# Optimization experiments

Measured on AMD Instinct MI355X. Metric: run time of the kernel, lower is better.

Reference implementation:

```python
import jax, jax.numpy as jnp
import numpy as np

TOP_K = 2


def setup_inputs() -> dict:
    key = jax.random.key(0)
    k1, k2, k3, k4 = jax.random.split(key, 4)
    B, N, D, E, F = 4, 2048, 1024, 8, 4096
    x = jax.random.normal(k1, (B, N, D), dtype=jnp.float32)
    gate_w = jax.random.normal(k2, (D, E), dtype=jnp.float32) * (D ** -0.5)
    w1 = jax.random.normal(k3, (E, D, F), dtype=jnp.float32) * (D ** -0.5)
    w2 = jax.random.normal(k4, (E, F, D), dtype=jnp.float32) * (F ** -0.5)
    return {"x": x, "gate_w": gate_w, "w1": w1, "w2": w2}


def reference(x, gate_w, w1, w2):
    # x: (B, N, D); gate_w: (D, E); w1: (E, D, F); w2: (E, F, D)
    E = gate_w.shape[-1]
    gate_logits = jnp.einsum("bnd,de->bne", x, gate_w)
    gate_probs = jax.nn.softmax(gate_logits, axis=-1)          # (B, N, E)
    top_k_probs, top_k_idx = jax.lax.top_k(gate_probs, TOP_K)   # (B, N, K)
    top_k_weights = top_k_probs / jnp.sum(top_k_probs, axis=-1, keepdims=True)
    # combined per-expert weight: sum_k w_k * onehot(idx_k) -> (B, N, E)
    comb = jnp.sum(jax.nn.one_hot(top_k_idx, E, dtype=x.dtype)
                   * top_k_weights[..., None], axis=2)
    # dense all-expert FFN (matches the torch masked-dense math exactly)
    h = jax.nn.gelu(jnp.einsum("bnd,edf->benf", x, w1))         # (B, E, N, F)
    expert_out = jnp.einsum("benf,efd->bend", h, w2)            # (B, E, N, D)
    output = jnp.einsum("bne,bend->bnd", comb, expert_out)      # (B, N, D)
    return output
```

## Files before the change

### kernel.cpp

```cpp
#include <hip/hip_runtime.h>
#include <hip/hip_bf16.h>

typedef short s16x8 __attribute__((ext_vector_type(8)));
typedef float f32x4 __attribute__((ext_vector_type(4)));
typedef float f32x2 __attribute__((ext_vector_type(2)));
typedef unsigned short us8 __attribute__((ext_vector_type(8)));
typedef unsigned short us4 __attribute__((ext_vector_type(4)));

#define T_TOK 8192
#define DDIM 1024
#define NEXP 8
#define FDIM 4096
#define MAXT 72
#define PADMAX (16384 + NEXP * 256)

#define GLOAD16(dst, src) \
  __builtin_amdgcn_global_load_lds((const __attribute__((address_space(1))) unsigned int*)(src), \
                                   (__attribute__((address_space(3))) unsigned int*)(dst), 16, 0, 0)
#define WAITVM(n) asm volatile("s_waitcnt vmcnt(" #n ")" ::: "memory")
#define MEMFENCE asm volatile("" ::: "memory")

__device__ __forceinline__ float gelu_fast(float x) {
  float x2 = x * x;
  float t = x * fmaf(x2, -0.07135532f, -1.5957691f);
  float e = __expf(t);
  return x * __builtin_amdgcn_rcpf(1.0f + e);
}
__device__ __forceinline__ float bf2f(unsigned short v) {
  return __uint_as_float((unsigned)v << 16);
}

__global__ __launch_bounds__(256) void gate_kernel(
    const float* __restrict__ x, const float* __restrict__ gw,
    int* __restrict__ tok_e, float* __restrict__ tok_w)
{
  int lane = threadIdx.x & 63;
  int tok = blockIdx.x * 4 + (threadIdx.x >> 6);
  const float* xr = x + (size_t)tok * DDIM;
  float acc[NEXP];
#pragma unroll
  for (int e = 0; e < NEXP; ++e) acc[e] = 0.f;
  for (int i = 0; i < DDIM / 64; ++i) {
    int d = i * 64 + lane;
    float xv = xr[d];
    const float* g = gw + (size_t)d * NEXP;
#pragma unroll
    for (int e = 0; e < NEXP; ++e) acc[e] += xv * g[e];
  }
#pragma unroll
  for (int off = 32; off > 0; off >>= 1) {
#pragma unroll
    for (int e = 0; e < NEXP; ++e) acc[e] += __shfl_xor(acc[e], off);
  }
  if (lane == 0) {
    int i1 = 0; float m1 = acc[0];
#pragma unroll
    for (int e = 1; e < NEXP; ++e) if (acc[e] > m1) { m1 = acc[e]; i1 = e; }
    int i2 = -1; float m2 = -3.4e38f;
#pragma unroll
    for (int e = 0; e < NEXP; ++e) if (e != i1 && acc[e] > m2) { m2 = acc[e]; i2 = e; }
    float w1 = 1.f / (1.f + expf(m2 - m1));
    tok_e[tok * 2] = i1; tok_e[tok * 2 + 1] = i2;
    tok_w[tok * 2] = w1; tok_w[tok * 2 + 1] = 1.f - w1;
  }
}

__global__ __launch_bounds__(256) void count_kernel(
    const int* __restrict__ tok_e, int* __restrict__ counts)
{
  __shared__ int lc[NEXP];
  if (threadIdx.x < NEXP) lc[threadIdx.x] = 0;
  __syncthreads();
  int tok = blockIdx.x * 256 + threadIdx.x;
  atomicAdd(&lc[tok_e[tok * 2]], 1);
  atomicAdd(&lc[tok_e[tok * 2 + 1]], 1);
  __syncthreads();
  if (threadIdx.x < NEXP) atomicAdd(&counts[threadIdx.x], lc[threadIdx.x]);
}

__global__ void scan_kernel(const int* __restrict__ counts, int* padded_off,
                            int* tile_e, int* tile_row, int* numTiles,
                            int* __restrict__ pair_token)
{
  if (blockIdx.x == 0) {
    for (int i = threadIdx.x; i < PADMAX; i += 256) pair_token[i] = -1;
    if (threadIdx.x == 0) {
      int off = 0, a = 0;
      for (int e = 0; e < NEXP; ++e) {
        padded_off[e] = off;
        int c = counts[e];
        int nt = (c + 255) / 256;
        for (int i = 0; i < nt; ++i) { tile_e[a] = e; tile_row[a] = off + i * 256; ++a; }
        off += nt * 256;
      }
      *numTiles = a;
    }
  }
}

__global__ __launch_bounds__(256) void scatter_kernel(
    const int* __restrict__ tok_e, const int* __restrict__ padded_off,
    int* __restrict__ fill, int* __restrict__ pair_token, int* __restrict__ tok_slot)
{
  __shared__ int lc[NEXP], lbase[NEXP];
  if (threadIdx.x < NEXP) lc[threadIdx.x] = 0;
  __syncthreads();
  int tok = blockIdx.x * 256 + threadIdx.x;
  int e0 = tok_e[tok * 2], e1 = tok_e[tok * 2 + 1];
  int r0 = atomicAdd(&lc[e0], 1);
  int r1 = atomicAdd(&lc[e1], 1);
  __syncthreads();
  if (threadIdx.x < NEXP) lbase[threadIdx.x] = atomicAdd(&fill[threadIdx.x], lc[threadIdx.x]);
  __syncthreads();
  int s0 = padded_off[e0] + lbase[e0] + r0;
  int s1 = padded_off[e1] + lbase[e1] + r1;
  pair_token[s0] = tok;
  pair_token[s1] = tok;
  tok_slot[tok * 2] = s0;
  tok_slot[tok * 2 + 1] = s1;
}

__global__ __launch_bounds__(256) void gather_x(
    const float* __restrict__ x, const int* __restrict__ pair_token,
    __hip_bfloat16* __restrict__ Xg)
{
  int gid = blockIdx.x * 256 + threadIdx.x;
  int r = gid >> 7;
  int c = (gid & 127) << 3;
  if (r >= PADMAX) return;
  int tk = pair_token[r];
  __hip_bfloat16 v[8];
  if (tk < 0) {
#pragma unroll
    for (int j = 0; j < 8; ++j) v[j] = __float2bfloat16(0.f);
  } else {
    const float* src = x + (size_t)tk * DDIM + c;
    f32x4 a = __builtin_nontemporal_load((const f32x4*)src);
    f32x4 b = __builtin_nontemporal_load((const f32x4*)(src + 4));
#pragma unroll
    for (int j = 0; j < 4; ++j) v[j] = __float2bfloat16(a[j]);
#pragma unroll
    for (int j = 0; j < 4; ++j) v[4 + j] = __float2bfloat16(b[j]);
  }
  *(us8*)(Xg + (size_t)r * DDIM + c) = *(const us8*)v;
}

__global__ __launch_bounds__(256) void transpose_conv(
    const float* __restrict__ in, __hip_bfloat16* __restrict__ out, int R, int C)
{
  __shared__ __hip_bfloat16 tile[64][66];
  size_t mat = (size_t)R * C;
  const float* ip = in + (size_t)blockIdx.z * mat;
  __hip_bfloat16* op = out + (size_t)blockIdx.z * mat;
  int c0 = blockIdx.x * 64, r0 = blockIdx.y * 64;
  int tx = threadIdx.x & 31, ty = threadIdx.x >> 5;
#pragma unroll
  for (int i = 0; i < 8; ++i) {
    int r = r0 + ty + i * 8;
    f32x2 v = __builtin_nontemporal_load(
        (const f32x2*)(ip + (size_t)r * C + c0 + tx * 2));
    tile[ty + i * 8][tx * 2]     = __float2bfloat16(v[0]);
    tile[ty + i * 8][tx * 2 + 1] = __float2bfloat16(v[1]);
  }
  __syncthreads();
#pragma unroll
  for (int i = 0; i < 8; ++i) {
    int cc = c0 + ty + i * 8;
    __hip_bfloat16 a = tile[tx * 2][ty + i * 8];
    __hip_bfloat16 b = tile[tx * 2 + 1][ty + i * 8];
    unsigned short ua = *(unsigned short*)&a, ub = *(unsigned short*)&b;
    unsigned int packed = (unsigned)ua | ((unsigned)ub << 16);
    *(unsigned int*)(op + (size_t)cc * R + r0 + tx * 2) = packed;
  }
}

template<int LD, int NT, int LDO, int NCOL, int SC, bool GELU>
__global__ __launch_bounds__(512, 2) void moe_gemm8(
    const __hip_bfloat16* __restrict__ A, const __hip_bfloat16* __restrict__ B,
    __hip_bfloat16* __restrict__ Out,
    const int* __restrict__ tile_e, const int* __restrict__ tile_row,
    const int* __restrict__ numTiles)
{
  constexpr int STU = 3 * SC;
  constexpr int NCG = NCOL / SC;
  const int bid = blockIdx.x;
  const int xcd = bid & 7;
  const int idx = bid >> 3;
  const int stg = idx / STU;
  const int within = idx % STU;
  const int colg = stg % NCG;
  const int tg = stg / NCG;
  const int tl = tg * 3 + within % 3;
  const int col = colg * SC + within / 3;
  const int nT = *numTiles;
  const int tile = ((xcd * nT) >> 3) + tl;
  if (tile >= (((xcd + 1) * nT) >> 3)) return;

  __shared__ __align__(16) __hip_bfloat16 lds[8][8192];
  const int t = threadIdx.x, lane = t & 63, w = t >> 6;
  const int wm = w >> 2, wn = w & 3;
  const int fr = lane & 15, fkg = lane >> 4;
  const size_t rowoff = (size_t)(w * 8 + (lane >> 3)) * LD + (((lane & 7) ^ (lane >> 3)) << 3);
  const int aoff = (wm * 64 + fr) * 64;
  const int boff = (wn * 32 + fr) * 64;
  const int swk0 = (fkg ^ (fr & 7)) * 8;
  const int swk1 = ((4 + fkg) ^ (fr & 7)) * 8;

  const int e = tile_e[tile];
  const int row0 = tile_row[tile];
  const int col0 = col * 256;
  const __hip_bfloat16* Ab = A + (size_t)row0 * LD;
  const __hip_bfloat16* Bb = B + (size_t)e * ((size_t)FDIM * DDIM) + (size_t)col0 * LD;

  auto STAGEH = [&](const __hip_bfloat16* base, int mat, int half, int tt) {
    __hip_bfloat16* d = &lds[(((tt & 1) << 2) | (mat << 1) | half)][0] + w * 512;
    const __hip_bfloat16* s = base + (size_t)(half * 128) * LD + (size_t)tt * 64 + rowoff;
    GLOAD16(d, s);
    GLOAD16(d + 4096, s + (size_t)64 * LD);
  };

  f32x4 acc[4][4][2] = {};
  s16x8 af0[4][2], af1[4][2], b0[2][2], b1[2][2];

  STAGEH(Ab, 0, 0, 0); STAGEH(Bb, 1, 0, 0); STAGEH(Bb, 1, 1, 0); STAGEH(Ab, 0, 1, 0);
  STAGEH(Ab, 0, 0, 1);
  WAITVM(6);
  __builtin_amdgcn_s_barrier();
  MEMFENCE;
  {
    const __hip_bfloat16* A0r = &lds[0][0];
    const __hip_bfloat16* B0r = &lds[2][0];
#pragma unroll
    for (int m = 0; m < 4; ++m) {
      af0[m][0] = *(const s16x8*)(A0r + aoff + m * 1024 + swk0);
      af0[m][1] = *(const s16x8*)(A0r + aoff + m * 1024 + swk1);
    }
#pragma unroll
    for (int n = 0; n < 2; ++n) {
      b0[n][0] = *(const s16x8*)(B0r + boff + n * 1024 + swk0);
      b0[n][1] = *(const s16x8*)(B0r + boff + n * 1024 + swk1);
    }
  }

  for (int kt = 0; kt < NT; ++kt) {
    const int buf = kt & 1;
    const bool p1 = (kt + 1) < NT;
    const bool p2 = (kt + 2) < NT;
    const __hip_bfloat16* A1r = &lds[(buf << 2) | 1][0];
    const __hip_bfloat16* B1r = &lds[(buf << 2) | 3][0];
    const __hip_bfloat16* A0n = &lds[((buf ^ 1) << 2) | 0][0];
    const __hip_bfloat16* B0n = &lds[((buf ^ 1) << 2) | 2][0];

    if (p1) STAGEH(Bb, 1, 0, kt + 1);
    if (p1) { WAITVM(6); } else { WAITVM(2); }
    __builtin_amdgcn_s_barrier();
    MEMFENCE;
#pragma unroll
    for (int n = 0; n < 2; ++n) {
      b1[n][0] = *(const s16x8*)(B1r + boff + n * 1024 + swk0);
      b1[n][1] = *(const s16x8*)(B1r + boff + n * 1024 + swk1);
    }
    __builtin_amdgcn_s_setprio(1);
#pragma unroll
    for (int kk = 0; kk < 2; ++kk)
#pragma unroll
      for (int m = 0; m < 4; ++m)
#pragma unroll
        for (int n = 0; n < 2; ++n)
          acc[0][m][n] = __builtin_amdgcn_mfma_f32_16x16x32_bf16(af0[m][kk], b0[n][kk], acc[0][m][n], 0, 0, 0);
    __builtin_amdgcn_s_setprio(0);
    MEMFENCE;

    if (p1) STAGEH(Bb, 1, 1, kt + 1);
    if (p1) { WAITVM(6); } else { WAITVM(0); }
    __builtin_amdgcn_s_barrier();
    MEMFENCE;
#pragma unroll
    for (int m = 0; m < 4; ++m) {
      af1[m][0] = *(const s16x8*)(A1r + aoff + m * 1024 + swk0);
      af1[m][1] = *(const s16x8*)(A1r + aoff + m * 1024 + swk1);
    }
    __builtin_amdgcn_s_setprio(1);
#pragma unroll
    for (int kk = 0; kk < 2; ++kk)
#pragma unroll
      for (int m = 0; m < 4; ++m)
#pragma unroll
        for (int n = 0; n < 2; ++n)
          acc[1][m][n] = __builtin_amdgcn_mfma_f32_16x16x32_bf16(af0[m][kk], b1[n][kk], acc[1][m][n], 0, 0, 0);
    __builtin_amdgcn_s_setprio(0);
    MEMFENCE;

    if (p1) STAGEH(Ab, 0, 1, kt + 1);
    __builtin_amdgcn_s_barrier();
    MEMFENCE;
    __builtin_amdgcn_s_setprio(1);
#pragma unroll
    for (int kk = 0; kk < 2; ++kk)
#pragma unroll
      for (int m = 0; m < 4; ++m)
#pragma unroll
        for (int n = 0; n < 2; ++n)
          acc[3][m][n] = __builtin_amdgcn_mfma_f32_16x16x32_bf16(af1[m][kk], b0[n][kk], acc[3][m][n], 0, 0, 0);
    __builtin_amdgcn_s_setprio(0);
    MEMFENCE;

    if (p2) STAGEH(Ab, 0, 0, kt + 2);
    if (p1) { if (p2) { WAITVM(6); } else { WAITVM(4); } }
    __builtin_amdgcn_s_barrier();
    MEMFENCE;
    if (p1) {
#pragma unroll
      for (int m = 0; m < 4; ++m) {
        af0[m][0] = *(const s16x8*)(A0n + aoff + m * 1024 + swk0);
        af0[m][1] = *(const s16x8*)(A0n + aoff + m * 1024 + swk1);
      }
#pragma unroll
      for (int n = 0; n < 2; ++n) {
        b0[n][0] = *(const s16x8*)(B0n + boff + n * 1024 + swk0);
        b0[n][1] = *(const s16x8*)(B0n + boff + n * 1024 + swk1);
      }
    }
    __builtin_amdgcn_s_setprio(1);
#pragma unroll
    for (int kk = 0; kk < 2; ++kk)
#pragma unroll
      for (int m = 0; m < 4; ++m)
#pragma unroll
        for (int n = 0; n < 2; ++n)
          acc[2][m][n] = __builtin_amdgcn_mfma_f32_16x16x32_bf16(af1[m][kk], b1[n][kk], acc[2][m][n], 0, 0, 0);
    __builtin_amdgcn_s_setprio(0);
    MEMFENCE;
  }

  const int cbase = col0 + wn * 32 + fr;
#pragma unroll
  for (int mh = 0; mh < 2; ++mh) {
    const int qa = mh ? 3 : 0;
    const int qb = mh ? 2 : 1;
#pragma unroll
    for (int m = 0; m < 4; ++m) {
#pragma unroll
      for (int j = 0; j < 4; ++j) {
        int r = row0 + mh * 128 + wm * 64 + m * 16 + fkg * 4 + j;
        __hip_bfloat16* p = Out + (size_t)r * LDO + cbase;
        float v0 = acc[qa][m][0][j];
        float v1 = acc[qa][m][1][j];
        float v2 = acc[qb][m][0][j];
        float v3 = acc[qb][m][1][j];
        if (GELU) {
          v0 = gelu_fast(v0); v1 = gelu_fast(v1);
          v2 = gelu_fast(v2); v3 = gelu_fast(v3);
        }
        p[0]   = __float2bfloat16(v0);
        p[16]  = __float2bfloat16(v1);
        p[128] = __float2bfloat16(v2);
        p[144] = __float2bfloat16(v3);
      }
    }
  }
}

__global__ __launch_bounds__(256) void combine_kernel(
    const __hip_bfloat16* __restrict__ Eout, const int* __restrict__ tok_slot,
    const float* __restrict__ tok_w, float* __restrict__ out)
{
  int tok = blockIdx.x;
  int sa = tok_slot[tok * 2], sb = tok_slot[tok * 2 + 1];
  float wa = tok_w[tok * 2], wb = tok_w[tok * 2 + 1];
  const __hip_bfloat16* ra = Eout + (size_t)sa * DDIM;
  const __hip_bfloat16* rb = Eout + (size_t)sb * DDIM;
  float* op = out + (size_t)tok * DDIM;
  int c = threadIdx.x * 4;
  us4 va = *(const us4*)(ra + c);
  us4 vb = *(const us4*)(rb + c);
  float4 o;
  o.x = wa * bf2f(va.x) + wb * bf2f(vb.x);
  o.y = wa * bf2f(va.y) + wb * bf2f(vb.y);
  o.z = wa * bf2f(va.z) + wb * bf2f(vb.z);
  o.w = wa * bf2f(va.w) + wb * bf2f(vb.w);
  *(float4*)(op + c) = o;
}

extern "C" void kernel_launch(void* const* d_in, const int* in_sizes, int n_in,
                              void* d_out, int out_size, void* d_ws, size_t ws_size,
                              hipStream_t stream)
{
  const float* x      = (const float*)d_in[0];
  const float* gate_w = (const float*)d_in[1];
  const float* w1     = (const float*)d_in[2];
  const float* w2     = (const float*)d_in[3];
  float* out = (float*)d_out;

  char* ws = (char*)d_ws;
  size_t off = 0;
  auto alloc = [&](size_t bytes) -> void* {
    void* p = ws + off;
    off = (off + bytes + 255) & ~(size_t)255;
    return p;
  };
  int* ctrl = (int*)alloc(1024);
  int* counts     = ctrl + 0;
  int* fill       = ctrl + 8;
  int* padded_off = ctrl + 16;
  int* numTiles   = ctrl + 24;
  int*   tile_e     = (int*)alloc(MAXT * 4);
  int*   tile_row   = (int*)alloc(MAXT * 4);
  int*   tok_e      = (int*)alloc((size_t)T_TOK * 2 * 4);
  float* tok_w      = (float*)alloc((size_t)T_TOK * 2 * 4);
  int*   tok_slot   = (int*)alloc((size_t)T_TOK * 2 * 4);
  int*   pair_token = (int*)alloc((size_t)PADMAX * 4);
  __hip_bfloat16* XgEout = (__hip_bfloat16*)alloc((size_t)PADMAX * DDIM * 2);
  __hip_bfloat16* W1t  = (__hip_bfloat16*)alloc((size_t)NEXP * FDIM * DDIM * 2);
  __hip_bfloat16* W2t  = (__hip_bfloat16*)alloc((size_t)NEXP * FDIM * DDIM * 2);
  __hip_bfloat16* Hbuf = (__hip_bfloat16*)alloc((size_t)PADMAX * FDIM * 2);
  (void)in_sizes; (void)n_in; (void)ws_size; (void)out_size;

  (void)hipMemsetAsync(d_ws, 0, 1024, stream);

  gate_kernel<<<T_TOK / 4, 256, 0, stream>>>(x, gate_w, tok_e, tok_w);
  count_kernel<<<T_TOK / 256, 256, 0, stream>>>(tok_e, counts);
  scan_kernel<<<1, 256, 0, stream>>>(counts, padded_off, tile_e, tile_row, numTiles,
                                     pair_token);
  scatter_kernel<<<T_TOK / 256, 256, 0, stream>>>(tok_e, padded_off, fill,
                                                  pair_token, tok_slot);
  gather_x<<<(PADMAX * (DDIM / 8) + 255) / 256, 256, 0, stream>>>(x, pair_token, XgEout);

  transpose_conv<<<dim3(FDIM / 64, DDIM / 64, NEXP), 256, 0, stream>>>(w1, W1t, DDIM, FDIM);

  moe_gemm8<DDIM, DDIM / 64, FDIM, FDIM / 256, 8, true>
      <<<MAXT * (FDIM / 256), 512, 0, stream>>>(XgEout, W1t, Hbuf,
                                                tile_e, tile_row, numTiles);

  transpose_conv<<<dim3(DDIM / 64, FDIM / 64, NEXP), 256, 0, stream>>>(w2, W2t, FDIM, DDIM);

  moe_gemm8<FDIM, FDIM / 64, DDIM, DDIM / 256, 4, false>
      <<<MAXT * (DDIM / 256), 512, 0, stream>>>(Hbuf, W2t, XgEout,
                                                tile_e, tile_row, numTiles);

  combine_kernel<<<T_TOK, 256, 0, stream>>>(XgEout, tok_slot, tok_w, out);
}
```

Before: 485.8 us.

## Fuse weight transposes into gather and first GEMM launches to overlap work

The w1 transpose/convert is merged into the gather kernel as extra blocks, and the w2 transpose is appended as extra blocks to the first expert GEMM launch (two 64x64 tiles per 512-thread block, reusing its LDS). This removes two kernel launches and lets the memory-bound transposes run alongside the gather and the compute-bound GEMM1. The tradeoff is that the extra transpose blocks compete with GEMM1 blocks for CUs, and the xcd-based tile mapping depends on block ordering.

```diff
diff --git a/kernel.cpp b/kernel.cpp
--- a/kernel.cpp
+++ b/kernel.cpp
@@ -13,6 +13,9 @@
 #define FDIM 4096
 #define MAXT 72
 #define PADMAX (16384 + NEXP * 256)
+#define GATHB ((PADMAX * 128) / 256)
+#define TR1B 8192
+#define TR2B 4096
 
 #define GLOAD16(dst, src) \
   __builtin_amdgcn_global_load_lds((const __attribute__((address_space(1))) unsigned int*)(src), \
@@ -28,6 +31,31 @@
 }
 __device__ __forceinline__ float bf2f(unsigned short v) {
   return __uint_as_float((unsigned)v << 16);
+}
+
+__device__ __forceinline__ void trans64(const float* __restrict__ ip,
+                                        __hip_bfloat16* __restrict__ op,
+                                        int R, int C, int c0, int r0, int tid,
+                                        __hip_bfloat16 (*tile)[66]) {
+  int tx = tid & 31, ty = tid >> 5;
+#pragma unroll
+  for (int i = 0; i < 8; ++i) {
+    int r = r0 + ty + i * 8;
+    f32x2 v = __builtin_nontemporal_load(
+        (const f32x2*)(ip + (size_t)r * C + c0 + tx * 2));
+    tile[ty + i * 8][tx * 2]     = __float2bfloat16(v[0]);
+    tile[ty + i * 8][tx * 2 + 1] = __float2bfloat16(v[1]);
+  }
+  __syncthreads();
+#pragma unroll
+  for (int i = 0; i < 8; ++i) {
+    int cc = c0 + ty + i * 8;
+    __hip_bfloat16 a = tile[tx * 2][ty + i * 8];
+    __hip_bfloat16 b = tile[tx * 2 + 1][ty + i * 8];
+    unsigned short ua = *(unsigned short*)&a, ub = *(unsigned short*)&b;
+    unsigned int packed = (unsigned)ua | ((unsigned)ub << 16);
+    *(unsigned int*)(op + (size_t)cc * R + r0 + tx * 2) = packed;
+  }
 }
 
 __global__ __launch_bounds__(256) void gate_kernel(
@@ -120,11 +148,22 @@
   tok_slot[tok * 2 + 1] = s1;
 }
 
-__global__ __launch_bounds__(256) void gather_x(
+__global__ __launch_bounds__(256) void gather_trans1(
     const float* __restrict__ x, const int* __restrict__ pair_token,
-    __hip_bfloat16* __restrict__ Xg)
-{
-  int gid = blockIdx.x * 256 + threadIdx.x;
+    __hip_bfloat16* __restrict__ Xg,
+    const float* __restrict__ w1, __hip_bfloat16* __restrict__ W1t)
+{
+  __shared__ __hip_bfloat16 tile[64][66];
+  int bid = blockIdx.x;
+  if (bid >= GATHB) {
+    int i = bid - GATHB;
+    int xq = i & 63, yq = (i >> 6) & 15, z = i >> 10;
+    size_t mat = (size_t)DDIM * FDIM;
+    trans64(w1 + (size_t)z * mat, W1t + (size_t)z * mat,
+            DDIM, FDIM, xq * 64, yq * 64, threadIdx.x, tile);
+    return;
+  }
+  int gid = bid * 256 + threadIdx.x;
   int r = gid >> 7;
   int c = (gid & 127) << 3;
   if (r >= PADMAX) return;
@@ -145,42 +184,26 @@
   *(us8*)(Xg + (size_t)r * DDIM + c) = *(const us8*)v;
 }
 
-__global__ __launch_bounds__(256) void transpose_conv(
-    const float* __restrict__ in, __hip_bfloat16* __restrict__ out, int R, int C)
-{
-  __shared__ __hip_bfloat16 tile[64][66];
-  size_t mat = (size_t)R * C;
-  const float* ip = in + (size_t)blockIdx.z * mat;
-  __hip_bfloat16* op = out + (size_t)blockIdx.z * mat;
-  int c0 = blockIdx.x * 64, r0 = blockIdx.y * 64;
-  int tx = threadIdx.x & 31, ty = threadIdx.x >> 5;
-#pragma unroll
-  for (int i = 0; i < 8; ++i) {
-    int r = r0 + ty + i * 8;
-    f32x2 v = __builtin_nontemporal_load(
-        (const f32x2*)(ip + (size_t)r * C + c0 + tx * 2));
-    tile[ty + i * 8][tx * 2]     = __float2bfloat16(v[0]);
-    tile[ty + i * 8][tx * 2 + 1] = __float2bfloat16(v[1]);
-  }
-  __syncthreads();
-#pragma unroll
-  for (int i = 0; i < 8; ++i) {
-    int cc = c0 + ty + i * 8;
-    __hip_bfloat16 a = tile[tx * 2][ty + i * 8];
-    __hip_bfloat16 b = tile[tx * 2 + 1][ty + i * 8];
-    unsigned short ua = *(unsigned short*)&a, ub = *(unsigned short*)&b;
-    unsigned int packed = (unsigned)ua | ((unsigned)ub << 16);
-    *(unsigned int*)(op + (size_t)cc * R + r0 + tx * 2) = packed;
-  }
-}
-
-template<int LD, int NT, int LDO, int NCOL, int SC, bool GELU>
+template<int LD, int NT, int LDO, int NCOL, int SC, bool GELU, bool FUSET>
 __global__ __launch_bounds__(512, 2) void moe_gemm8(
     const __hip_bfloat16* __restrict__ A, const __hip_bfloat16* __restrict__ B,
     __hip_bfloat16* __restrict__ Out,
     const int* __restrict__ tile_e, const int* __restrict__ tile_row,
-    const int* __restrict__ numTiles)
-{
+    const int* __restrict__ numTiles,
+    const float* __restrict__ w2, __hip_bfloat16* __restrict__ W2t)
+{
+  __shared__ __align__(16) __hip_bfloat16 lds[8][8192];
+  if (FUSET && (int)blockIdx.x >= MAXT * NCOL) {
+    int i2 = ((int)blockIdx.x - MAXT * NCOL) * 2 + (threadIdx.x >> 8);
+    int xq = i2 & 15, yq = (i2 >> 4) & 63, z = i2 >> 10;
+    int sub = threadIdx.x >> 8, tid = threadIdx.x & 255;
+    __hip_bfloat16 (*tile)[66] =
+        reinterpret_cast<__hip_bfloat16(*)[66]>(&lds[0][0] + sub * 64 * 66);
+    size_t mat = (size_t)FDIM * DDIM;
+    trans64(w2 + (size_t)z * mat, W2t + (size_t)z * mat,
+            FDIM, DDIM, xq * 64, yq * 64, tid, tile);
+    return;
+  }
   constexpr int STU = 3 * SC;
   constexpr int NCG = NCOL / SC;
   const int bid = blockIdx.x;
@@ -196,7 +219,6 @@
   const int tile = ((xcd * nT) >> 3) + tl;
   if (tile >= (((xcd + 1) * nT) >> 3)) return;
 
-  __shared__ __align__(16) __hip_bfloat16 lds[8][8192];
   const int t = threadIdx.x, lane = t & 63, w = t >> 6;
   const int wm = w >> 2, wn = w & 3;
   const int fr = lane & 15, fkg = lane >> 4;
@@ -424,19 +446,16 @@
                                      pair_token);
   scatter_kernel<<<T_TOK / 256, 256, 0, stream>>>(tok_e, padded_off, fill,
                                                   pair_token, tok_slot);
-  gather_x<<<(PADMAX * (DDIM / 8) + 255) / 256, 256, 0, stream>>>(x, pair_token, XgEout);
-
-  transpose_conv<<<dim3(FDIM / 64, DDIM / 64, NEXP), 256, 0, stream>>>(w1, W1t, DDIM, FDIM);
-
-  moe_gemm8<DDIM, DDIM / 64, FDIM, FDIM / 256, 8, true>
-      <<<MAXT * (FDIM / 256), 512, 0, stream>>>(XgEout, W1t, Hbuf,
-                                                tile_e, tile_row, numTiles);
-
-  transpose_conv<<<dim3(DDIM / 64, FDIM / 64, NEXP), 256, 0, stream>>>(w2, W2t, FDIM, DDIM);
-
-  moe_gemm8<FDIM, FDIM / 64, DDIM, DDIM / 256, 4, false>
+  gather_trans1<<<GATHB + TR1B, 256, 0, stream>>>(x, pair_token, XgEout, w1, W1t);
+
+  moe_gemm8<DDIM, DDIM / 64, FDIM, FDIM / 256, 8, true, true>
+      <<<MAXT * (FDIM / 256) + TR2B, 512, 0, stream>>>(XgEout, W1t, Hbuf,
+                                                       tile_e, tile_row, numTiles,
+                                                       w2, W2t);
+  moe_gemm8<FDIM, FDIM / 64, DDIM, DDIM / 256, 4, false, false>
       <<<MAXT * (DDIM / 256), 512, 0, stream>>>(Hbuf, W2t, XgEout,
-                                                tile_e, tile_row, numTiles);
+                                                tile_e, tile_row, numTiles,
+                                                nullptr, nullptr);
 
   combine_kernel<<<T_TOK, 256, 0, stream>>>(XgEout, tok_slot, tok_w, out);
 }
```

Result: faster. 472.3 us (-2.8%).
